# Kernel tuning notes

Measured on AMD Instinct MI355X. Metric: run time of the kernel, lower is better.

The kernel has to match this reference:

```python
import jax, jax.numpy as jnp
import numpy as np
import math

B, S, HID, H = 4, 1024, 1024, 16
DH = HID // H

def setup_inputs() -> dict:
    key = jax.random.key(0)
    ks = jax.random.split(key, 16)
    inp = {
        'q': jax.random.normal(ks[0], (B, S, HID), jnp.float32),
        'k': jax.random.normal(ks[1], (B, S, HID), jnp.float32),
        'v': jax.random.normal(ks[2], (B, S, HID), jnp.float32),
        'k_b': jax.random.normal(ks[3], (B, S, HID), jnp.float32),
        'mask': jax.random.randint(ks[4], (B, S), 0, 2, jnp.int32),
    }
    sc = 1.0 / math.sqrt(HID)
    names = ['Wq', 'Wk', 'Wv', 'Wkb', 'Wo']
    for i, n in enumerate(names):
        inp[n] = jax.random.normal(ks[5 + i], (HID, HID), jnp.float32) * sc
        inp['b' + n[1:]] = jnp.zeros((HID,), jnp.float32)
    return inp

def _split_heads(x):
    # [B,S,HID] -> [B,H,S,DH]
    return x.reshape(B, S, H, DH).transpose(0, 2, 1, 3)

def reference(q, k, v, k_b, mask, Wq, bq, Wk, bk, Wv, bv, Wkb, bkb, Wo, bo):
    qh = _split_heads(q @ Wq.T + bq)
    kh = _split_heads(k @ Wk.T + bk)
    vh = _split_heads(v @ Wv.T + bv)
    kbh = _split_heads(k_b @ Wkb.T + bkb)
    scale = 1.0 / math.sqrt(3 * DH)
    # Q@K^T + Q@Kb^T == Q@(K+Kb)^T
    corr = jnp.einsum('bhsd,bhtd->bhst', qh, kh + kbh) * scale
    # mask[b,j] broadcast over heads and query positions
    corr = jnp.where(mask[:, None, None, :] == 0, jnp.float32(-1e9), corr)
    prob = jax.nn.softmax(corr, axis=-1)  # dropout p=0 (eval)
    hidden = jnp.einsum('bhst,bhtd->bhsd', prob, vh)
    hidden = hidden.transpose(0, 2, 1, 3).reshape(B, S, HID)
    return hidden @ Wo.T + bo
```

## Files before the change

### kernel.cpp

```cpp
#include <hip/hip_runtime.h>
#include <hip/hip_bf16.h>
#include <stdint.h>

#define B_   4
#define S_   1024
#define HID_ 1024
#define H_   16
#define DH_  64

typedef short bf16x8 __attribute__((ext_vector_type(8)));
typedef float f32x4  __attribute__((ext_vector_type(4)));
typedef unsigned int u32;
typedef unsigned short u16;

typedef u32 __attribute__((address_space(1))) as1_u32;
typedef u32 __attribute__((address_space(3))) as3_u32;

__device__ __forceinline__ f32x4 mfma16(bf16x8 a, bf16x8 b, f32x4 c) {
  return __builtin_amdgcn_mfma_f32_16x16x32_bf16(a, b, c, 0, 0, 0);
}

__device__ __forceinline__ void gload16(const void* g, void* l) {
  __builtin_amdgcn_global_load_lds((const as1_u32*)g, (as3_u32*)l, 16, 0, 0);
}

__device__ __forceinline__ u16 f2bf(float f) {
  __hip_bfloat16 h = __float2bfloat16(f);
  union { __hip_bfloat16 h; u16 u; } cv; cv.h = h; return cv.u;
}

__device__ __forceinline__ u32 cvtpk(float lo, float hi) {
  u32 r;
  asm("v_cvt_pk_bf16_f32 %0, %1, %2" : "=v"(r) : "v"(lo), "v"(hi));
  return r;
}

__global__ __launch_bounds__(256) void cvt_acts(const float* a0, const float* a1,
                                                const float* a2, const float* a3,
                                                u16* d0, u16* d1, u16* d2, u16* d3) {
  int t = blockIdx.x * 256 + threadIdx.x;
  int sel = t >> 19;
  size_t i = (size_t)(t & 524287) * 8;
  const float* s; u16* d;
  if (sel == 0)      { s = a0; d = d0; }
  else if (sel == 1) { s = a1; d = d1; }
  else if (sel == 2) { s = a2; d = d2; }
  else               { s = a3; d = d3; }
  float4 v0 = *(const float4*)(s + i);
  float4 v1 = *(const float4*)(s + i + 4);
  uint4 r;
  r.x = (u32)f2bf(v0.x) | ((u32)f2bf(v0.y) << 16);
  r.y = (u32)f2bf(v0.z) | ((u32)f2bf(v0.w) << 16);
  r.z = (u32)f2bf(v1.x) | ((u32)f2bf(v1.y) << 16);
  r.w = (u32)f2bf(v1.z) | ((u32)f2bf(v1.w) << 16);
  *(uint4*)(d + i) = r;
}

__global__ __launch_bounds__(256) void cvt_wts(const float* a0, const float* a1,
                                               const float* a2, const float* a3, const float* a4,
                                               u16* d0, u16* d1, u16* d2, u16* d3, u16* d4) {
  int t = blockIdx.x * 256 + threadIdx.x;
  int sel = t >> 17;
  size_t i = (size_t)(t & 131071) * 8;
  const float* s; u16* d;
  if (sel == 0)      { s = a0; d = d0; }
  else if (sel == 1) { s = a1; d = d1; }
  else if (sel == 2) { s = a2; d = d2; }
  else if (sel == 3) { s = a3; d = d3; }
  else               { s = a4; d = d4; }
  float4 v0 = *(const float4*)(s + i);
  float4 v1 = *(const float4*)(s + i + 4);
  uint4 r;
  r.x = (u32)f2bf(v0.x) | ((u32)f2bf(v0.y) << 16);
  r.y = (u32)f2bf(v0.z) | ((u32)f2bf(v0.w) << 16);
  r.z = (u32)f2bf(v1.x) | ((u32)f2bf(v1.y) << 16);
  r.w = (u32)f2bf(v1.z) | ((u32)f2bf(v1.w) << 16);
  *(uint4*)(d + i) = r;
}

__global__ __launch_bounds__(256) void gemm_proj(
    const u16* __restrict__ qbf, const u16* __restrict__ Wqbf,
    const u16* __restrict__ kbf, const u16* __restrict__ Wkbf,
    const u16* __restrict__ kbbf, const u16* __restrict__ Wkbbf,
    const u16* __restrict__ vbf, const u16* __restrict__ Wvbf,
    const float* __restrict__ bq, const float* __restrict__ bk,
    const float* __restrict__ bkb, const float* __restrict__ bv,
    u16* __restrict__ Qp, u16* __restrict__ KKp, u16* __restrict__ Vtp) {
  __shared__ __align__(16) char smem[32768];
  const int tid = threadIdx.x;
  const int lane = tid & 63, w = tid >> 6;
  const int g = lane >> 4, ql = lane & 15;
  const int wm = w >> 1, wn = w & 1;
  const int unit = blockIdx.x >> 8;
  const int bidu = blockIdx.x & 255;
  const int m0 = (bidu >> 3) * 128;
  const int n0 = (bidu & 7) * 128;
  const int xr = ql & 7;

  const u16 *A0, *W0, *A1, *W1;
  const float *b0, *b1;
  int nkt; float osc;
  if (unit == 0) { A0 = kbf; W0 = Wkbf; A1 = kbbf; W1 = Wkbbf; b0 = bk; b1 = bkb; nkt = 32; osc = 1.f; }
  else if (unit == 1) { A0 = qbf; W0 = Wqbf; A1 = qbf; W1 = Wqbf; b0 = bq; b1 = nullptr; nkt = 16;
                        osc = 0.07216878364870322f * 1.44269504088896340f; }
  else { A0 = vbf; W0 = Wvbf; A1 = vbf; W1 = Wvbf; b0 = bv; b1 = nullptr; nkt = 16; osc = 1.f; }

  f32x4 acc[4][4];
  #pragma unroll
  for (int mi = 0; mi < 4; ++mi)
    #pragma unroll
    for (int ni = 0; ni < 4; ++ni) acc[mi][ni] = f32x4{0.f, 0.f, 0.f, 0.f};

  for (int kt = 0; kt < nkt; ++kt) {
    const u16* As = (kt >= 16) ? A1 : A0;
    const u16* Ws = (kt >= 16) ? W1 : W0;
    const int kk = (kt & 15) * 64;
    #pragma unroll
    for (int is = 0; is < 4; ++is) {
      int o = is * 4096 + tid * 16;
      int row = o >> 7, ch = (o >> 4) & 7;
      gload16(As + (size_t)(m0 + row) * HID_ + kk + ((ch ^ (row & 7)) * 8),
              smem + is * 4096 + w * 1024);
      gload16(Ws + (size_t)(n0 + row) * HID_ + kk + ((ch ^ (row & 7)) * 8),
              smem + 16384 + is * 4096 + w * 1024);
    }
    __syncthreads();

    bf16x8 af[4][2], bfv[4][2];
    #pragma unroll
    for (int mi = 0; mi < 4; ++mi)
      #pragma unroll
      for (int c = 0; c < 2; ++c) {
        int row = wm * 64 + mi * 16 + ql;
        af[mi][c] = *(const bf16x8*)(smem + row * 128 + (((c * 4 + g) ^ xr) * 16));
      }
    #pragma unroll
    for (int ni = 0; ni < 4; ++ni)
      #pragma unroll
      for (int c = 0; c < 2; ++c) {
        int row = wn * 64 + ni * 16 + ql;
        bfv[ni][c] = *(const bf16x8*)(smem + 16384 + row * 128 + (((c * 4 + g) ^ xr) * 16));
      }
    #pragma unroll
    for (int c = 0; c < 2; ++c)
      #pragma unroll
      for (int mi = 0; mi < 4; ++mi)
        #pragma unroll
        for (int ni = 0; ni < 4; ++ni)
          acc[mi][ni] = mfma16(af[mi][c], bfv[ni][c], acc[mi][ni]);
    __syncthreads();
  }

  if (unit != 2) {
    u16* outp = (unit == 0) ? KKp : Qp;
    #pragma unroll
    for (int ni = 0; ni < 4; ++ni) {
      int n = n0 + wn * 64 + ni * 16 + ql;
      float bs = b0[n];
      if (unit == 0) bs += b1[n];
      #pragma unroll
      for (int mi = 0; mi < 4; ++mi)
        #pragma unroll
        for (int i = 0; i < 4; ++i) {
          int m = m0 + wm * 64 + mi * 16 + g * 4 + i;
          outp[(size_t)m * HID_ + n] = f2bf((acc[mi][ni][i] + bs) * osc);
        }
    }
  } else {
    char* tp = smem + w * 8192;
    #pragma unroll
    for (int ni = 0; ni < 4; ++ni) {
      int n = n0 + wn * 64 + ni * 16 + ql;
      float bs = b0[n];
      #pragma unroll
      for (int mi = 0; mi < 4; ++mi)
        #pragma unroll
        for (int i = 0; i < 4; ++i) {
          int nl = ni * 16 + ql;
          int ml = mi * 16 + g * 4 + i;
          *(u16*)(tp + nl * 128 + (((ml >> 3) ^ (nl & 7)) * 16) + (ml & 7) * 2) =
              f2bf(acc[mi][ni][i] + bs);
        }
    }
    __syncthreads();
    int nl = lane;
    int n = n0 + wn * 64 + nl;
    int h = n >> 6, dh = n & 63;
    int mb = m0 + wm * 64;
    int b = mb >> 10, s0 = mb & 1023;
    int bh = b * H_ + h;
    u16* orow = Vtp + (((size_t)(bh * DH_ + dh)) << 10) + s0;
    #pragma unroll
    for (int j = 0; j < 8; ++j) {
      uint4 val = *(const uint4*)(tp + nl * 128 + ((j ^ (nl & 7)) * 16));
      *(uint4*)(orow + j * 8) = val;
    }
  }
}

__global__ __launch_bounds__(256) void gemm_o(const u16* __restrict__ A0, const u16* __restrict__ W0,
                                              const float* __restrict__ bias0, float* __restrict__ outp) {
  __shared__ __align__(16) char smem[24576];
  const int tid = threadIdx.x;
  const int lane = tid & 63, w = tid >> 6;
  const int g = lane >> 4, ql = lane & 15;
  const int wm = w >> 1, wn = w & 1;
  const int bid = blockIdx.x;
  const int m0 = (bid >> 4) * 128;
  const int n0 = (bid & 15) * 64;
  const int xr = ql & 7;

  f32x4 acc[4][2];
  #pragma unroll
  for (int mi = 0; mi < 4; ++mi)
    #pragma unroll
    for (int ni = 0; ni < 2; ++ni) acc[mi][ni] = f32x4{0.f, 0.f, 0.f, 0.f};

  for (int kt = 0; kt < 16; ++kt) {
    const int kk = kt * 64;
    #pragma unroll
    for (int is = 0; is < 4; ++is) {
      int o = is * 4096 + tid * 16;
      int row = o >> 7, ch = (o >> 4) & 7;
      gload16(A0 + (size_t)(m0 + row) * HID_ + kk + ((ch ^ (row & 7)) * 8),
              smem + is * 4096 + w * 1024);
    }
    #pragma unroll
    for (int is = 0; is < 2; ++is) {
      int o = is * 4096 + tid * 16;
      int row = o >> 7, ch = (o >> 4) & 7;
      gload16(W0 + (size_t)(n0 + row) * HID_ + kk + ((ch ^ (row & 7)) * 8),
              smem + 16384 + is * 4096 + w * 1024);
    }
    __syncthreads();

    bf16x8 af[4][2], bfv[2][2];
    #pragma unroll
    for (int mi = 0; mi < 4; ++mi)
      #pragma unroll
      for (int c = 0; c < 2; ++c) {
        int row = wm * 64 + mi * 16 + ql;
        af[mi][c] = *(const bf16x8*)(smem + row * 128 + (((c * 4 + g) ^ xr) * 16));
      }
    #pragma unroll
    for (int ni = 0; ni < 2; ++ni)
      #pragma unroll
      for (int c = 0; c < 2; ++c) {
        int row = wn * 32 + ni * 16 + ql;
        bfv[ni][c] = *(const bf16x8*)(smem + 16384 + row * 128 + (((c * 4 + g) ^ xr) * 16));
      }
    #pragma unroll
    for (int c = 0; c < 2; ++c)
      #pragma unroll
      for (int mi = 0; mi < 4; ++mi)
        #pragma unroll
        for (int ni = 0; ni < 2; ++ni)
          acc[mi][ni] = mfma16(af[mi][c], bfv[ni][c], acc[mi][ni]);
    __syncthreads();
  }

  #pragma unroll
  for (int ni = 0; ni < 2; ++ni) {
    int n = n0 + wn * 32 + ni * 16 + ql;
    float bs = bias0[n];
    #pragma unroll
    for (int mi = 0; mi < 4; ++mi)
      #pragma unroll
      for (int i = 0; i < 4; ++i) {
        int m = m0 + wm * 64 + mi * 16 + g * 4 + i;
        outp[(size_t)m * HID_ + n] = acc[mi][ni][i] + bs;
      }
  }
}

__global__ __launch_bounds__(256, 4) void attn(const u16* __restrict__ Qp, const u16* __restrict__ KKp,
                                               const u16* __restrict__ Vt, const int* __restrict__ mask,
                                               u16* __restrict__ hidden) {
  __shared__ __align__(16) char smem[40960];
  const int tid = threadIdx.x;
  const int lane = tid & 63, w = tid >> 6;
  const int g = lane >> 4, ql = lane & 15;
  const int bid = blockIdx.x;
  const int bh = (bid & 7) * 8 + ((bid >> 3) & 7);
  const int qt = bid >> 6;
  const int b = bh >> 4, h = bh & 15;
  const int q0 = qt * 64;
  const int xr = ql & 7;

  #pragma unroll
  for (int is = 0; is < 2; ++is) {
    int o = is * 4096 + tid * 16;
    int row = o >> 7, ch = (o >> 4) & 7;
    gload16(KKp + (size_t)(b * S_ + row) * HID_ + h * DH_ + ((ch ^ (row & 7)) * 8),
            smem + is * 4096 + w * 1024);
    gload16(Vt + (size_t)(bh * DH_ + row) * S_ + ((ch ^ (row & 7)) * 8),
            smem + 8192 + is * 4096 + w * 1024);
  }

  const u16* qrow = Qp + (size_t)(b * S_ + q0 + w * 16 + ql) * HID_ + h * DH_;
  bf16x8 qb0 = *(const bf16x8*)(qrow + g * 8);
  bf16x8 qb1 = *(const bf16x8*)(qrow + 32 + g * 8);
  const int* maskp = mask + b * S_;

  f32x4 oacc[4];
  #pragma unroll
  for (int d = 0; d < 4; ++d) oacc[d] = f32x4{0.f, 0.f, 0.f, 0.f};
  float m_run = -1e30f, l_run = 0.f;
  char* pbase = smem + 32768 + w * 2048 + ql * 128;

  __syncthreads();

  int pb = 0;
  for (int it = 0; it < 16; ++it) {
    if (it < 15) {
      const int k0s = (it + 1) * 64;
      const int bo = (pb ^ 1) * 16384;
      #pragma unroll
      for (int is = 0; is < 2; ++is) {
        int o = is * 4096 + tid * 16;
        int row = o >> 7, ch = (o >> 4) & 7;
        gload16(KKp + (size_t)(b * S_ + k0s + row) * HID_ + h * DH_ + ((ch ^ (row & 7)) * 8),
                smem + bo + is * 4096 + w * 1024);
        gload16(Vt + (size_t)(bh * DH_ + row) * S_ + k0s + ((ch ^ (row & 7)) * 8),
                smem + bo + 8192 + is * 4096 + w * 1024);
      }
    }
    const char* kb_ = smem + pb * 16384;
    const char* vb_ = smem + pb * 16384 + 8192;
    const int k0 = it * 64;

    float sv[4][4];
    #pragma unroll
    for (int t = 0; t < 4; ++t) {
      int4 mv = *(const int4*)(maskp + k0 + 16 * t + 4 * g);
      const char* krow = kb_ + (16 * t + ql) * 128;
      bf16x8 ka0 = *(const bf16x8*)(krow + ((g ^ xr) * 16));
      bf16x8 ka1 = *(const bf16x8*)(krow + (((4 + g) ^ xr) * 16));
      f32x4 st = mfma16(ka0, qb0, f32x4{0.f, 0.f, 0.f, 0.f});
      st = mfma16(ka1, qb1, st);
      sv[t][0] = mv.x ? st[0] : -1e9f;
      sv[t][1] = mv.y ? st[1] : -1e9f;
      sv[t][2] = mv.z ? st[2] : -1e9f;
      sv[t][3] = mv.w ? st[3] : -1e9f;
    }
    float mloc = sv[0][0];
    #pragma unroll
    for (int t = 0; t < 4; ++t)
      #pragma unroll
      for (int i = 0; i < 4; ++i) mloc = fmaxf(mloc, sv[t][i]);
    mloc = fmaxf(mloc, __shfl_xor(mloc, 16, 64));
    mloc = fmaxf(mloc, __shfl_xor(mloc, 32, 64));
    if (__any(mloc > m_run + 10.f)) {
      float mnew = fmaxf(m_run, mloc);
      float alpha = __builtin_amdgcn_exp2f(m_run - mnew);
      l_run *= alpha;
      #pragma unroll
      for (int d = 0; d < 4; ++d) oacc[d] *= alpha;
      m_run = mnew;
    }
    float rsum = 0.f;
    float pvs[4][4];
    #pragma unroll
    for (int t = 0; t < 4; ++t)
      #pragma unroll
      for (int i = 0; i < 4; ++i) {
        float p = __builtin_amdgcn_exp2f(sv[t][i] - m_run);
        pvs[t][i] = p; rsum += p;
      }
    rsum += __shfl_xor(rsum, 16, 64);
    rsum += __shfl_xor(rsum, 32, 64);
    l_run += rsum;

    #pragma unroll
    for (int t = 0; t < 4; ++t) {
      uint2 pw;
      pw.x = cvtpk(pvs[t][0], pvs[t][1]);
      pw.y = cvtpk(pvs[t][2], pvs[t][3]);
      *(uint2*)(pbase + (((4 * t + g) ^ (2 * xr)) * 8)) = pw;
    }
    #pragma unroll
    for (int c = 0; c < 2; ++c) {
      bf16x8 pf = *(const bf16x8*)(pbase + (((c * 4 + g) ^ xr) * 16));
      #pragma unroll
      for (int d = 0; d < 4; ++d) {
        bf16x8 va = *(const bf16x8*)(vb_ + (16 * d + ql) * 128 + (((c * 4 + g) ^ xr) * 16));
        oacc[d] = mfma16(va, pf, oacc[d]);
      }
    }
    __syncthreads();
    pb ^= 1;
  }

  float inv = 1.0f / l_run;
  char* ep = smem + w * 2304;
  #pragma unroll
  for (int d = 0; d < 4; ++d)
    #pragma unroll
    for (int i = 0; i < 4; ++i)
      *(u16*)(ep + ql * 144 + (16 * d + 4 * g + i) * 2) = f2bf(oacc[d][i] * inv);
  __syncthreads();
  int r = lane >> 2, cc = lane & 3;
  const char* erow = smem + w * 2304 + r * 144 + cc * 32;
  uint4 v0 = *(const uint4*)erow;
  uint4 v1 = *(const uint4*)(erow + 16);
  u16* orow = hidden + (size_t)(b * S_ + q0 + w * 16 + r) * HID_ + h * DH_ + cc * 16;
  *(uint4*)orow = v0;
  *(uint4*)(orow + 8) = v1;
}

extern "C" void kernel_launch(void* const* d_in, const int* in_sizes, int n_in,
                              void* d_out, int out_size, void* d_ws, size_t ws_size,
                              hipStream_t stream) {
  (void)in_sizes; (void)n_in; (void)out_size; (void)ws_size;
  const float* q    = (const float*)d_in[0];
  const float* k    = (const float*)d_in[1];
  const float* v    = (const float*)d_in[2];
  const float* kb   = (const float*)d_in[3];
  const int*   mask = (const int*)  d_in[4];
  const float* Wq   = (const float*)d_in[5];
  const float* bq   = (const float*)d_in[6];
  const float* Wk   = (const float*)d_in[7];
  const float* bk   = (const float*)d_in[8];
  const float* Wv   = (const float*)d_in[9];
  const float* bv   = (const float*)d_in[10];
  const float* Wkb  = (const float*)d_in[11];
  const float* bkb  = (const float*)d_in[12];
  const float* Wo   = (const float*)d_in[13];
  const float* bo   = (const float*)d_in[14];

  char* ws = (char*)d_ws;
  const size_t MB = 1024 * 1024;
  u16* qbf   = (u16*)(ws + 0 * MB);
  u16* kbf   = (u16*)(ws + 8 * MB);
  u16* vbf   = (u16*)(ws + 16 * MB);
  u16* kbbf  = (u16*)(ws + 24 * MB);
  u16* Wqbf  = (u16*)(ws + 32 * MB);
  u16* Wkbf  = (u16*)(ws + 34 * MB);
  u16* Wvbf  = (u16*)(ws + 36 * MB);
  u16* Wkbbf = (u16*)(ws + 38 * MB);
  u16* Wobf  = (u16*)(ws + 40 * MB);
  u16* Qp    = (u16*)(ws + 42 * MB);
  u16* KKp   = (u16*)(ws + 50 * MB);
  u16* Vtp   = (u16*)(ws + 58 * MB);
  u16* hid   = (u16*)(ws + 66 * MB);

  cvt_acts<<<8192, 256, 0, stream>>>(q, k, v, kb, qbf, kbf, vbf, kbbf);
  cvt_wts<<<2560, 256, 0, stream>>>(Wq, Wk, Wv, Wkb, Wo, Wqbf, Wkbf, Wvbf, Wkbbf, Wobf);
  gemm_proj<<<768, 256, 0, stream>>>(qbf, Wqbf, kbf, Wkbf, kbbf, Wkbbf, vbf, Wvbf,
                                     bq, bk, bkb, bv, Qp, KKp, Vtp);
  attn<<<1024, 256, 0, stream>>>(Qp, KKp, Vtp, mask, hid);
  gemm_o<<<512, 256, 0, stream>>>(hid, Wobf, bo, (float*)d_out);
}
```

Before: 130.3 us.

## Fuse conversion kernels, rebalance projection grid, remap blocks, refine attention sync

Result: faster. 127.2 us (-2.4%).

```diff
diff --git a/kernel.cpp b/kernel.cpp
--- a/kernel.cpp
+++ b/kernel.cpp
@@ -35,46 +35,38 @@
   return r;
 }
 
-__global__ __launch_bounds__(256) void cvt_acts(const float* a0, const float* a1,
-                                                const float* a2, const float* a3,
-                                                u16* d0, u16* d1, u16* d2, u16* d3) {
-  int t = blockIdx.x * 256 + threadIdx.x;
-  int sel = t >> 19;
-  size_t i = (size_t)(t & 524287) * 8;
-  const float* s; u16* d;
-  if (sel == 0)      { s = a0; d = d0; }
-  else if (sel == 1) { s = a1; d = d1; }
-  else if (sel == 2) { s = a2; d = d2; }
-  else               { s = a3; d = d3; }
+__global__ __launch_bounds__(256) void cvt_all(
+    const float* a0, const float* a1, const float* a2, const float* a3,
+    const float* w0, const float* w1, const float* w2, const float* w3, const float* w4,
+    u16* da0, u16* da1, u16* da2, u16* da3,
+    u16* dw0, u16* dw1, u16* dw2, u16* dw3, u16* dw4) {
+  int bb = blockIdx.x;
+  const float* s; u16* d; size_t i;
+  if (bb < 8192) {
+    int t = bb * 256 + threadIdx.x;
+    int sel = t >> 19;
+    i = (size_t)(t & 524287) * 8;
+    if (sel == 0)      { s = a0; d = da0; }
+    else if (sel == 1) { s = a1; d = da1; }
+    else if (sel == 2) { s = a2; d = da2; }
+    else               { s = a3; d = da3; }
+  } else {
+    int t = (bb - 8192) * 256 + threadIdx.x;
+    int sel = t >> 17;
+    i = (size_t)(t & 131071) * 8;
+    if (sel == 0)      { s = w0; d = dw0; }
+    else if (sel == 1) { s = w1; d = dw1; }
+    else if (sel == 2) { s = w2; d = dw2; }
+    else if (sel == 3) { s = w3; d = dw3; }
+    else               { s = w4; d = dw4; }
+  }
   float4 v0 = *(const float4*)(s + i);
   float4 v1 = *(const float4*)(s + i + 4);
   uint4 r;
-  r.x = (u32)f2bf(v0.x) | ((u32)f2bf(v0.y) << 16);
-  r.y = (u32)f2bf(v0.z) | ((u32)f2bf(v0.w) << 16);
-  r.z = (u32)f2bf(v1.x) | ((u32)f2bf(v1.y) << 16);
-  r.w = (u32)f2bf(v1.z) | ((u32)f2bf(v1.w) << 16);
-  *(uint4*)(d + i) = r;
-}
-
-__global__ __launch_bounds__(256) void cvt_wts(const float* a0, const float* a1,
-                                               const float* a2, const float* a3, const float* a4,
-                                               u16* d0, u16* d1, u16* d2, u16* d3, u16* d4) {
-  int t = blockIdx.x * 256 + threadIdx.x;
-  int sel = t >> 17;
-  size_t i = (size_t)(t & 131071) * 8;
-  const float* s; u16* d;
-  if (sel == 0)      { s = a0; d = d0; }
-  else if (sel == 1) { s = a1; d = d1; }
-  else if (sel == 2) { s = a2; d = d2; }
-  else if (sel == 3) { s = a3; d = d3; }
-  else               { s = a4; d = d4; }
-  float4 v0 = *(const float4*)(s + i);
-  float4 v1 = *(const float4*)(s + i + 4);
-  uint4 r;
-  r.x = (u32)f2bf(v0.x) | ((u32)f2bf(v0.y) << 16);
-  r.y = (u32)f2bf(v0.z) | ((u32)f2bf(v0.w) << 16);
-  r.z = (u32)f2bf(v1.x) | ((u32)f2bf(v1.y) << 16);
-  r.w = (u32)f2bf(v1.z) | ((u32)f2bf(v1.w) << 16);
+  r.x = cvtpk(v0.x, v0.y);
+  r.y = cvtpk(v0.z, v0.w);
+  r.z = cvtpk(v1.x, v1.y);
+  r.w = cvtpk(v1.z, v1.w);
   *(uint4*)(d + i) = r;
 }
 
@@ -91,19 +83,84 @@
   const int lane = tid & 63, w = tid >> 6;
   const int g = lane >> 4, ql = lane & 15;
   const int wm = w >> 1, wn = w & 1;
-  const int unit = blockIdx.x >> 8;
-  const int bidu = blockIdx.x & 255;
+  const int xr = ql & 7;
+  const int logical = (blockIdx.x & 7) * 128 + (blockIdx.x >> 3);
+
+  if (logical < 512) {
+    const int m0 = (logical >> 4) * 128;
+    const int n0 = (logical & 15) * 64;
+    f32x4 acc[4][2];
+    #pragma unroll
+    for (int mi = 0; mi < 4; ++mi)
+      #pragma unroll
+      for (int ni = 0; ni < 2; ++ni) acc[mi][ni] = f32x4{0.f, 0.f, 0.f, 0.f};
+
+    for (int kt = 0; kt < 32; ++kt) {
+      const u16* As = (kt < 16) ? kbf : kbbf;
+      const u16* Ws = (kt < 16) ? Wkbf : Wkbbf;
+      const int kk = (kt & 15) * 64;
+      #pragma unroll
+      for (int is = 0; is < 4; ++is) {
+        int o = is * 4096 + tid * 16;
+        int row = o >> 7, ch = (o >> 4) & 7;
+        gload16(As + (size_t)(m0 + row) * HID_ + kk + ((ch ^ (row & 7)) * 8),
+                smem + is * 4096 + w * 1024);
+      }
+      #pragma unroll
+      for (int is = 0; is < 2; ++is) {
+        int o = is * 4096 + tid * 16;
+        int row = o >> 7, ch = (o >> 4) & 7;
+        gload16(Ws + (size_t)(n0 + row) * HID_ + kk + ((ch ^ (row & 7)) * 8),
+                smem + 16384 + is * 4096 + w * 1024);
+      }
+      __syncthreads();
+      bf16x8 af[4][2], bfv[2][2];
+      #pragma unroll
+      for (int mi = 0; mi < 4; ++mi)
+        #pragma unroll
+        for (int c = 0; c < 2; ++c) {
+          int row = wm * 64 + mi * 16 + ql;
+          af[mi][c] = *(const bf16x8*)(smem + row * 128 + (((c * 4 + g) ^ xr) * 16));
+        }
+      #pragma unroll
+      for (int ni = 0; ni < 2; ++ni)
+        #pragma unroll
+        for (int c = 0; c < 2; ++c) {
+          int row = wn * 32 + ni * 16 + ql;
+          bfv[ni][c] = *(const bf16x8*)(smem + 16384 + row * 128 + (((c * 4 + g) ^ xr) * 16));
+        }
+      #pragma unroll
+      for (int c = 0; c < 2; ++c)
+        #pragma unroll
+        for (int mi = 0; mi < 4; ++mi)
+          #pragma unroll
+          for (int ni = 0; ni < 2; ++ni)
+            acc[mi][ni] = mfma16(af[mi][c], bfv[ni][c], acc[mi][ni]);
+      __syncthreads();
+    }
+    #pragma unroll
+    for (int ni = 0; ni < 2; ++ni) {
+      int n = n0 + wn * 32 + ni * 16 + ql;
+      float bs = bk[n] + bkb[n];
+      #pragma unroll
+      for (int mi = 0; mi < 4; ++mi)
+        #pragma unroll
+        for (int i = 0; i < 4; ++i) {
+          int m = m0 + wm * 64 + mi * 16 + g * 4 + i;
+          KKp[(size_t)m * HID_ + n] = f2bf(acc[mi][ni][i] + bs);
+        }
+    }
+    return;
+  }
+
+  const int unit = (logical - 512) >> 8;
+  const int bidu = logical & 255;
   const int m0 = (bidu >> 3) * 128;
   const int n0 = (bidu & 7) * 128;
-  const int xr = ql & 7;
-
-  const u16 *A0, *W0, *A1, *W1;
-  const float *b0, *b1;
-  int nkt; float osc;
-  if (unit == 0) { A0 = kbf; W0 = Wkbf; A1 = kbbf; W1 = Wkbbf; b0 = bk; b1 = bkb; nkt = 32; osc = 1.f; }
-  else if (unit == 1) { A0 = qbf; W0 = Wqbf; A1 = qbf; W1 = Wqbf; b0 = bq; b1 = nullptr; nkt = 16;
-                        osc = 0.07216878364870322f * 1.44269504088896340f; }
-  else { A0 = vbf; W0 = Wvbf; A1 = vbf; W1 = Wvbf; b0 = bv; b1 = nullptr; nkt = 16; osc = 1.f; }
+  const u16* A0 = unit ? vbf : qbf;
+  const u16* W0 = unit ? Wvbf : Wqbf;
+  const float* b0 = unit ? bv : bq;
+  const float osc = unit ? 1.f : 0.07216878364870322f * 1.44269504088896340f;
 
   f32x4 acc[4][4];
   #pragma unroll
@@ -111,21 +168,18 @@
     #pragma unroll
     for (int ni = 0; ni < 4; ++ni) acc[mi][ni] = f32x4{0.f, 0.f, 0.f, 0.f};
 
-  for (int kt = 0; kt < nkt; ++kt) {
-    const u16* As = (kt >= 16) ? A1 : A0;
-    const u16* Ws = (kt >= 16) ? W1 : W0;
-    const int kk = (kt & 15) * 64;
+  for (int kt = 0; kt < 16; ++kt) {
+    const int kk = kt * 64;
     #pragma unroll
     for (int is = 0; is < 4; ++is) {
       int o = is * 4096 + tid * 16;
       int row = o >> 7, ch = (o >> 4) & 7;
-      gload16(As + (size_t)(m0 + row) * HID_ + kk + ((ch ^ (row & 7)) * 8),
+      gload16(A0 + (size_t)(m0 + row) * HID_ + kk + ((ch ^ (row & 7)) * 8),
               smem + is * 4096 + w * 1024);
-      gload16(Ws + (size_t)(n0 + row) * HID_ + kk + ((ch ^ (row & 7)) * 8),
+      gload16(W0 + (size_t)(n0 + row) * HID_ + kk + ((ch ^ (row & 7)) * 8),
               smem + 16384 + is * 4096 + w * 1024);
     }
     __syncthreads();
-
     bf16x8 af[4][2], bfv[4][2];
     #pragma unroll
     for (int mi = 0; mi < 4; ++mi)
@@ -151,19 +205,17 @@
     __syncthreads();
   }
 
-  if (unit != 2) {
-    u16* outp = (unit == 0) ? KKp : Qp;
+  if (unit == 0) {
     #pragma unroll
     for (int ni = 0; ni < 4; ++ni) {
       int n = n0 + wn * 64 + ni * 16 + ql;
       float bs = b0[n];
-      if (unit == 0) bs += b1[n];
       #pragma unroll
       for (int mi = 0; mi < 4; ++mi)
         #pragma unroll
         for (int i = 0; i < 4; ++i) {
           int m = m0 + wm * 64 + mi * 16 + g * 4 + i;
-          outp[(size_t)m * HID_ + n] = f2bf((acc[mi][ni][i] + bs) * osc);
+          Qp[(size_t)m * HID_ + n] = f2bf((acc[mi][ni][i] + bs) * osc);
         }
     }
   } else {
@@ -205,9 +257,9 @@
   const int lane = tid & 63, w = tid >> 6;
   const int g = lane >> 4, ql = lane & 15;
   const int wm = w >> 1, wn = w & 1;
-  const int bid = blockIdx.x;
-  const int m0 = (bid >> 4) * 128;
-  const int n0 = (bid & 15) * 64;
+  const int logical = (blockIdx.x & 7) * 64 + (blockIdx.x >> 3);
+  const int m0 = (logical >> 4) * 128;
+  const int n0 = (logical & 15) * 64;
   const int xr = ql & 7;
 
   f32x4 acc[4][2];
@@ -233,7 +285,6 @@
               smem + 16384 + is * 4096 + w * 1024);
     }
     __syncthreads();
-
     bf16x8 af[4][2], bfv[2][2];
     #pragma unroll
     for (int mi = 0; mi < 4; ++mi)
@@ -308,12 +359,15 @@
   float m_run = -1e30f, l_run = 0.f;
   char* pbase = smem + 32768 + w * 2048 + ql * 128;
 
-  __syncthreads();
-
   int pb = 0;
   for (int it = 0; it < 16; ++it) {
+    const int k0 = it * 64;
+    int4 mv[4];
+    #pragma unroll
+    for (int t = 0; t < 4; ++t) mv[t] = *(const int4*)(maskp + k0 + 16 * t + 4 * g);
+    __builtin_amdgcn_sched_barrier(0);
     if (it < 15) {
-      const int k0s = (it + 1) * 64;
+      const int k0s = k0 + 64;
       const int bo = (pb ^ 1) * 16384;
       #pragma unroll
       for (int is = 0; is < 2; ++is) {
@@ -324,24 +378,27 @@
         gload16(Vt + (size_t)(bh * DH_ + row) * S_ + k0s + ((ch ^ (row & 7)) * 8),
                 smem + bo + 8192 + is * 4096 + w * 1024);
       }
-    }
+      asm volatile("s_waitcnt vmcnt(4)" ::: "memory");
+    } else {
+      asm volatile("s_waitcnt vmcnt(0)" ::: "memory");
+    }
+    __builtin_amdgcn_s_barrier();
+
     const char* kb_ = smem + pb * 16384;
     const char* vb_ = smem + pb * 16384 + 8192;
-    const int k0 = it * 64;
 
     float sv[4][4];
     #pragma unroll
     for (int t = 0; t < 4; ++t) {
-      int4 mv = *(const int4*)(maskp + k0 + 16 * t + 4 * g);
       const char* krow = kb_ + (16 * t + ql) * 128;
       bf16x8 ka0 = *(const bf16x8*)(krow + ((g ^ xr) * 16));
       bf16x8 ka1 = *(const bf16x8*)(krow + (((4 + g) ^ xr) * 16));
       f32x4 st = mfma16(ka0, qb0, f32x4{0.f, 0.f, 0.f, 0.f});
       st = mfma16(ka1, qb1, st);
-      sv[t][0] = mv.x ? st[0] : -1e9f;
-      sv[t][1] = mv.y ? st[1] : -1e9f;
-      sv[t][2] = mv.z ? st[2] : -1e9f;
-      sv[t][3] = mv.w ? st[3] : -1e9f;
+      sv[t][0] = mv[t].x ? st[0] : -1e9f;
+      sv[t][1] = mv[t].y ? st[1] : -1e9f;
+      sv[t][2] = mv[t].z ? st[2] : -1e9f;
+      sv[t][3] = mv[t].w ? st[3] : -1e9f;
     }
     float mloc = sv[0][0];
     #pragma unroll
@@ -387,7 +444,7 @@
         oacc[d] = mfma16(va, pf, oacc[d]);
       }
     }
-    __syncthreads();
+    __builtin_amdgcn_s_barrier();
     pb ^= 1;
   }
 
@@ -444,10 +501,10 @@
   u16* Vtp   = (u16*)(ws + 58 * MB);
   u16* hid   = (u16*)(ws + 66 * MB);
 
-  cvt_acts<<<8192, 256, 0, stream>>>(q, k, v, kb, qbf, kbf, vbf, kbbf);
-  cvt_wts<<<2560, 256, 0, stream>>>(Wq, Wk, Wv, Wkb, Wo, Wqbf, Wkbf, Wvbf, Wkbbf, Wobf);
-  gemm_proj<<<768, 256, 0, stream>>>(qbf, Wqbf, kbf, Wkbf, kbbf, Wkbbf, vbf, Wvbf,
-                                     bq, bk, bkb, bv, Qp, KKp, Vtp);
+  cvt_all<<<10752, 256, 0, stream>>>(q, k, v, kb, Wq, Wk, Wv, Wkb, Wo,
+                                     qbf, kbf, vbf, kbbf, Wqbf, Wkbf, Wvbf, Wkbbf, Wobf);
+  gemm_proj<<<1024, 256, 0, stream>>>(qbf, Wqbf, kbf, Wkbf, kbbf, Wkbbf, vbf, Wvbf,
+                                      bq, bk, bkb, bv, Qp, KKp, Vtp);
   attn<<<1024, 256, 0, stream>>>(Qp, KKp, Vtp, mask, hid);
   gemm_o<<<512, 256, 0, stream>>>(hid, Wobf, bo, (float*)d_out);
 }
```
